# Optimization experiments

Hardware: AMD Instinct MI355X
Metric: run time of the kernel (lower is better)

Reference implementation:

```python
import jax, jax.numpy as jnp
import numpy as np

SPATIAL_SHAPES = np.array([[100, 100], [50, 50], [25, 25], [13, 13]], dtype=np.int64)
LEVEL_START = np.concatenate([[0], np.cumsum(SPATIAL_SHAPES[:, 0] * SPATIAL_SHAPES[:, 1])[:-1]])
L_TOK = int((SPATIAL_SHAPES[:, 0] * SPATIAL_SHAPES[:, 1]).sum())  # 13294
B, D_MODEL, N_HEADS, N_LEVELS, N_POINTS, D_FFN = 4, 256, 8, 4, 4, 1024
HEAD_DIM = D_MODEL // N_HEADS


def setup_inputs() -> dict:
    key = jax.random.key(0)
    ks = jax.random.split(key, 16)
    p = lambda k, s: jax.random.normal(k, s, jnp.float32) * 0.02
    return {
        'src': jax.random.normal(ks[0], (B, L_TOK, D_MODEL), jnp.float32),
        'src2': jax.random.normal(ks[1], (B, L_TOK, D_MODEL), jnp.float32),
        'pos': jax.random.normal(ks[2], (B, L_TOK, D_MODEL), jnp.float32),
        'memory_pos': jax.random.normal(ks[3], (B, L_TOK, D_MODEL), jnp.float32),
        'value_w': p(ks[4], (D_MODEL, D_MODEL)), 'value_b': jnp.zeros((D_MODEL,), jnp.float32),
        'off_w': p(ks[5], (D_MODEL, N_HEADS * N_LEVELS * N_POINTS * 2)),
        'off_b': p(ks[6], (N_HEADS * N_LEVELS * N_POINTS * 2,)),
        'aw_w': p(ks[7], (D_MODEL, N_HEADS * N_LEVELS * N_POINTS)),
        'aw_b': jnp.zeros((N_HEADS * N_LEVELS * N_POINTS,), jnp.float32),
        'out_w': p(ks[8], (D_MODEL, D_MODEL)), 'out_b': jnp.zeros((D_MODEL,), jnp.float32),
        'ln_g': jnp.ones((D_MODEL,), jnp.float32), 'ln_b': jnp.zeros((D_MODEL,), jnp.float32),
        'lin1_w': p(ks[9], (D_MODEL, D_FFN)), 'lin1_b': jnp.zeros((D_FFN,), jnp.float32),
        'lin2_w': p(ks[10], (D_FFN, D_MODEL)), 'lin2_b': jnp.zeros((D_MODEL,), jnp.float32),
    }


def _layer_norm(x, g, b, eps=1e-5):
    mu = jnp.mean(x, -1, keepdims=True)
    var = jnp.mean(jnp.square(x - mu), -1, keepdims=True)
    return (x - mu) * jax.lax.rsqrt(var + eps) * g + b


def _reference_points():
    # per get_reference_points: normalized (x, y) centers per src level -> [1, L_TOK, 1, 2]
    pts = []
    for H_, W_ in SPATIAL_SHAPES:
        ry, rx = np.meshgrid(np.linspace(0.5, H_ - 0.5, H_) / H_,
                             np.linspace(0.5, W_ - 0.5, W_) / W_, indexing='ij')
        pts.append(np.stack([rx.reshape(-1), ry.reshape(-1)], -1))
    return jnp.asarray(np.concatenate(pts, 0), jnp.float32)[None, :, None, :]


def _bilinear(value, loc, H_, W_):
    # value: [N, H*W, D]; loc: [N, S, 2] normalized in [0,1]
    # matches F.grid_sample(align_corners=False, padding_mode='zeros') with grid = 2*loc-1
    x = loc[..., 0] * W_ - 0.5
    y = loc[..., 1] * H_ - 0.5
    x0 = jnp.floor(x)
    y0 = jnp.floor(y)
    wx1 = x - x0
    wy1 = y - y0
    out = jnp.zeros(value.shape[:1] + loc.shape[1:2] + value.shape[2:], value.dtype)
    for dy, wy in ((0, 1.0 - wy1), (1, wy1)):
        for dx, wx in ((0, 1.0 - wx1), (1, wx1)):
            xi = x0 + dx
            yi = y0 + dy
            valid = (xi >= 0) & (xi < W_) & (yi >= 0) & (yi < H_)
            idx = (jnp.clip(yi, 0, H_ - 1) * W_ + jnp.clip(xi, 0, W_ - 1)).astype(jnp.int32)
            v = jnp.take_along_axis(value, idx[..., None], axis=1)
            out = out + v * (wx * wy * valid)[..., None]
    return out


def _ms_deform_attn(query, ref, memory, value_w, value_b, off_w, off_b, aw_w, aw_b, out_w, out_b):
    Bq, Lq = query.shape[0], query.shape[1]
    value = (memory @ value_w + value_b).reshape(Bq, -1, N_HEADS, HEAD_DIM)
    offs = (query @ off_w + off_b).reshape(Bq, Lq, N_HEADS, N_LEVELS, N_POINTS, 2)
    norm = jnp.asarray(SPATIAL_SHAPES[:, ::-1].copy(), jnp.float32)  # (W, H) per level
    loc = ref[:, :, None, :, None, :] + offs / norm[None, None, None, :, None, :]
    aw = jax.nn.softmax((query @ aw_w + aw_b).reshape(Bq, Lq, N_HEADS, N_LEVELS * N_POINTS), -1)
    aw = aw.reshape(Bq, Lq, N_HEADS, N_LEVELS, N_POINTS)
    acc = jnp.zeros((Bq, Lq, N_HEADS, HEAD_DIM), query.dtype)
    for l in range(N_LEVELS):
        H_, W_ = int(SPATIAL_SHAPES[l, 0]), int(SPATIAL_SHAPES[l, 1])
        s = int(LEVEL_START[l])
        v = value[:, s:s + H_ * W_].transpose(0, 2, 1, 3).reshape(Bq * N_HEADS, H_ * W_, HEAD_DIM)
        ll = loc[:, :, :, l].transpose(0, 2, 1, 3, 4).reshape(Bq * N_HEADS, Lq * N_POINTS, 2)
        samp = _bilinear(v, ll, H_, W_).reshape(Bq, N_HEADS, Lq, N_POINTS, HEAD_DIM)
        acc = acc + jnp.einsum('bhqpd,bqhp->bqhd', samp, aw[:, :, :, l])
    return acc.reshape(Bq, Lq, D_MODEL) @ out_w + out_b


def reference(src, src2, pos, memory_pos, value_w, value_b, off_w, off_b, aw_w, aw_b,
              out_w, out_b, ln_g, ln_b, lin1_w, lin1_b, lin2_w, lin2_b):
    ref = _reference_points()
    q = src + pos
    mem = src2 + memory_pos
    attn = _ms_deform_attn(q, ref, mem, value_w, value_b, off_w, off_b, aw_w, aw_b, out_w, out_b)
    # residual + norm2 (dropout is identity in eval)
    x = _layer_norm(src + attn, ln_g, ln_b)
    # FFN; note the original re-uses norm2 (it was assigned twice in __init__)
    ffn = jax.nn.relu(x @ lin1_w + lin1_b) @ lin2_w + lin2_b
    return _layer_norm(x + ffn, ln_g, ln_b)
```

## Files before the change

kernel.cpp:

```cpp
#include <hip/hip_runtime.h>
#include <math.h>

#define L_TOKN 13294
#define BATCHN 4
#define NTOK (BATCHN * L_TOKN)
#define NTOKP 53248
#define DMODEL 256
#define DFFN 1024

typedef __attribute__((ext_vector_type(8))) short short8;
typedef __attribute__((ext_vector_type(4))) float f32x4;
typedef __attribute__((ext_vector_type(2))) float f32x2;

__device__ __forceinline__ ushort f2b(float f) {
    uint u = __float_as_uint(f);
    u += 0x7fff + ((u >> 16) & 1);
    return (ushort)(u >> 16);
}
__device__ __forceinline__ float b2f(uint h) {
    return __uint_as_float(h << 16);
}

__global__ __launch_bounds__(256) void prep_k(
    const float* __restrict__ s1, const float* __restrict__ p1,
    const float* __restrict__ s2, const float* __restrict__ p2,
    ushort* __restrict__ o1, ushort* __restrict__ o2,
    const float* __restrict__ w0, const float* __restrict__ w1,
    const float* __restrict__ w2, const float* __restrict__ w3,
    const float* __restrict__ w4, const float* __restrict__ w5,
    ushort* __restrict__ wtb, int n4)
{
    int i = blockIdx.x * 256 + threadIdx.x;
    if (i < 2 * n4) {
        const float* a; const float* b; ushort* o; int j;
        if (i < n4) { a = s1; b = p1; o = o1; j = i; }
        else        { a = s2; b = p2; o = o2; j = i - n4; }
        float4 va = ((const float4*)a)[j];
        float4 vb = ((const float4*)b)[j];
        ushort4 r;
        r.x = f2b(va.x + vb.x); r.y = f2b(va.y + vb.y);
        r.z = f2b(va.z + vb.z); r.w = f2b(va.w + vb.w);
        ((ushort4*)o)[j] = r;
        return;
    }
    int i2 = i - 2 * n4;
    const float* w; int Nd; size_t off; int j;
    if      (i2 < 65536)  { w = w0; Nd = 256;  off = 0;      j = i2; }
    else if (i2 < 131072) { w = w1; Nd = 256;  off = 65536;  j = i2 - 65536; }
    else if (i2 < 163840) { w = w2; Nd = 128;  off = 131072; j = i2 - 131072; }
    else if (i2 < 229376) { w = w3; Nd = 256;  off = 163840; j = i2 - 163840; }
    else if (i2 < 491520) { w = w4; Nd = 1024; off = 229376; j = i2 - 229376; }
    else if (i2 < 753664) { w = w5; Nd = 256;  off = 491520; j = i2 - 491520; }
    else return;
    int Kd = (i2 < 491520) ? 256 : 1024;
    int k = j / Nd, n = j - k * Nd;
    wtb[off + (size_t)n * Kd + k] = f2b(w[j]);
}

__device__ __forceinline__ void gemm_core(
    const ushort* __restrict__ A, const ushort* __restrict__ Wt,
    const float* __restrict__ bias, const float* __restrict__ bias2,
    float* __restrict__ Cf, ushort* __restrict__ Cb,
    int M, int N, int K, int relu, int nsplit, int m0, int n0)
{
    __shared__ ushort lds[16384];

    const int t  = threadIdx.x;
    const int wv = t >> 6, ln_ = t & 63;
    const int wr = wv >> 1, wc = wv & 1;
    const int fr = ln_ & 15;
    const int kg = ln_ >> 4;

    f32x4 acc[4][4];
    #pragma unroll
    for (int i = 0; i < 4; i++)
        #pragma unroll
        for (int j = 0; j < 4; j++) acc[i][j] = (f32x4)0.0f;

    int aoff[4], boff[4];
    #pragma unroll
    for (int i = 0; i < 4; i++) {
        aoff[i] = (wr * 64 + i * 16 + fr) * 32 + kg * 8;
        boff[i] = 4096 + (wc * 64 + i * 16 + fr) * 32 + kg * 8;
    }

#define STAGE(pbuf, k0) do {                                                       \
    _Pragma("unroll")                                                              \
    for (int ii = 0; ii < 2; ii++) {                                               \
        int c = (wv * 2 + ii) * 64 + ln_;                                          \
        int m = c >> 2, s = c & 3;                                                 \
        const ushort* sa = A  + (size_t)(m0 + m) * K + (k0) + s * 8;               \
        const ushort* sb = Wt + (size_t)(n0 + m) * K + (k0) + s * 8;               \
        __builtin_amdgcn_global_load_lds(                                          \
            (const __attribute__((address_space(1))) unsigned int*)sa,             \
            (__attribute__((address_space(3))) unsigned int*)&lds[(pbuf) * 8192 + (wv * 2 + ii) * 512], \
            16, 0, 0);                                                             \
        __builtin_amdgcn_global_load_lds(                                          \
            (const __attribute__((address_space(1))) unsigned int*)sb,             \
            (__attribute__((address_space(3))) unsigned int*)&lds[(pbuf) * 8192 + 4096 + (wv * 2 + ii) * 512], \
            16, 0, 0);                                                             \
    }                                                                              \
} while (0)

    const int nk = K >> 5;
    STAGE(0, 0);
    if (nk > 1) STAGE(1, 32);

    for (int ks = 0; ks < nk; ks++) {
        const int p = ks & 1;
        if (ks + 1 < nk) {
            asm volatile("s_waitcnt vmcnt(4)" ::: "memory");
        } else {
            asm volatile("s_waitcnt vmcnt(0)" ::: "memory");
        }
        __builtin_amdgcn_s_barrier();
        __builtin_amdgcn_sched_barrier(0);

        short8 af[4], bf[4];
        const int pb = p * 8192;
        #pragma unroll
        for (int i = 0; i < 4; i++) {
            af[i] = *(const short8*)&lds[pb + aoff[i]];
            bf[i] = *(const short8*)&lds[pb + boff[i]];
        }
        if (ks + 2 < nk) {
            asm volatile("s_waitcnt lgkmcnt(0)" ::: "memory");
            __builtin_amdgcn_s_barrier();
            __builtin_amdgcn_sched_barrier(0);
            STAGE(p, (ks + 2) << 5);
        }
        #pragma unroll
        for (int i = 0; i < 4; i++)
            #pragma unroll
            for (int j = 0; j < 4; j++)
                acc[i][j] = __builtin_amdgcn_mfma_f32_16x16x32_bf16(af[i], bf[j], acc[i][j], 0, 0, 0);
    }
#undef STAGE

    #pragma unroll
    for (int i = 0; i < 4; i++) {
        #pragma unroll
        for (int j = 0; j < 4; j++) {
            int col = n0 + wc * 64 + j * 16 + fr;
            float bv = (col < nsplit) ? bias[col] : bias2[col - nsplit];
            #pragma unroll
            for (int e = 0; e < 4; e++) {
                int row = m0 + wr * 64 + i * 16 + kg * 4 + e;
                if (row >= M) continue;
                float v = acc[i][j][e] + bv;
                if (relu) v = fmaxf(v, 0.f);
                if (Cf) Cf[(size_t)row * N + col] = v;
                if (Cb) Cb[(size_t)row * N + col] = f2b(v);
            }
        }
    }
}

__global__ __launch_bounds__(256) void mgemm_k(
    const ushort* __restrict__ A, const ushort* __restrict__ Wt,
    const float* __restrict__ bias, const float* __restrict__ bias2,
    float* __restrict__ Cf, ushort* __restrict__ Cb,
    int M, int N, int K, int relu, int nsplit)
{
    gemm_core(A, Wt, bias, bias2, Cf, Cb, M, N, K, relu, nsplit,
              blockIdx.y * 128, blockIdx.x * 128);
}

__global__ __launch_bounds__(256) void projs_k(
    const ushort* __restrict__ memb, const ushort* __restrict__ qb,
    const ushort* __restrict__ value_wt, const ushort* __restrict__ offaw_wt,
    const float* __restrict__ value_b, const float* __restrict__ off_b,
    const float* __restrict__ aw_b,
    ushort* __restrict__ vb, ushort* __restrict__ offawb)
{
    const int x = blockIdx.x;
    const int m0 = blockIdx.y * 128;
    const ushort* A; const ushort* Wt; const float* b1; const float* b2;
    ushort* Cb; int N, n0;
    if (x < 2) { A = memb; Wt = value_wt; b1 = value_b; b2 = value_b;
                 Cb = vb; N = 256; n0 = x * 128; }
    else       { A = qb;   Wt = offaw_wt; b1 = off_b;   b2 = aw_b;
                 Cb = offawb; N = 384; n0 = (x - 2) * 128; }
    gemm_core(A, Wt, b1, b2, nullptr, Cb, NTOK, N, 256, 0, 256, m0, n0);
}

__global__ __launch_bounds__(256) void deform_k(
    const ushort* __restrict__ Vb,
    const ushort* __restrict__ OFFAW,
    ushort* __restrict__ OUTb)
{
    __shared__ uint4 pw_idx[4][2][136];
    __shared__ uint2 pw_w[4][2][136];

    const int t = threadIdx.x;
    const int wv = t >> 6, lane = t & 63;
    const int tok0 = blockIdx.x * 8 + wv * 2;

    const int HWc[4] = {100, 50, 25, 13};
    const int STc[4] = {0, 10000, 12500, 13125};

    const int ppb = lane & 15;
    const int lvb = ppb >> 2;
    #pragma unroll
    for (int it = 0; it < 4; it++) {
        int tk = it >> 1;
        int h  = ((it & 1) << 2) + (lane >> 4);
        int row = tok0 + tk;
        int b = row / L_TOKN;
        int l = row - b * L_TOKN;
        int st_q, Wq;
        if      (l < 10000) { st_q = 0;     Wq = 100; }
        else if (l < 12500) { st_q = 10000; Wq = 50;  }
        else if (l < 13125) { st_q = 12500; Wq = 25;  }
        else                { st_q = 13125; Wq = 13;  }
        int li = l - st_q;
        int rowi = li / Wq;
        int coli = li - rowi * Wq;
        float rx = (coli + 0.5f) / (float)Wq;
        float ry = (rowi + 0.5f) / (float)Wq;

        const size_t rbase = (size_t)row * 384;
        uint oxy = *(const uint*)(OFFAW + rbase + h * 32 + ppb * 2);
        float ox = b2f(oxy & 0xffffu);
        float oy = b2f(oxy >> 16);
        float lg = b2f((uint)OFFAW[rbase + 256 + h * 16 + ppb]);
        float mx = lg;
        #pragma unroll
        for (int o = 8; o; o >>= 1) mx = fmaxf(mx, __shfl_xor(mx, o));
        float ex = __expf(lg - mx);
        float sm = ex;
        #pragma unroll
        for (int o = 8; o; o >>= 1) sm += __shfl_xor(sm, o);
        float aw = ex / sm;

        int Wl = HWc[lvb], stl = STc[lvb];
        float Wlf = (float)Wl;
        float x = (rx + ox / Wlf) * Wlf - 0.5f;
        float y = (ry + oy / Wlf) * Wlf - 0.5f;
        float x0f = floorf(x), y0f = floorf(y);
        float wx1 = x - x0f, wy1 = y - y0f;
        float wx0 = 1.f - wx1, wy0 = 1.f - wy1;
        int x0 = (int)x0f, y0 = (int)y0f;
        bool vx0 = (x0 >= 0) & (x0 < Wl);
        bool vx1 = (x0 + 1 >= 0) & (x0 + 1 < Wl);
        bool vy0 = (y0 >= 0) & (y0 < Wl);
        bool vy1 = (y0 + 1 >= 0) & (y0 + 1 < Wl);
        int cx0 = min(max(x0, 0), Wl - 1), cx1 = min(max(x0 + 1, 0), Wl - 1);
        int cy0 = min(max(y0, 0), Wl - 1), cy1 = min(max(y0 + 1, 0), Wl - 1);
        uint gb = (uint)(b * L_TOKN + stl);
        uint4 o4;
        o4.x = (gb + cy0 * Wl + cx0) * 512u;
        o4.y = (gb + cy0 * Wl + cx1) * 512u;
        o4.z = (gb + cy1 * Wl + cx0) * 512u;
        o4.w = (gb + cy1 * Wl + cx1) * 512u;
        float w00 = wx0 * wy0 * aw * (float)(vx0 & vy0);
        float w10 = wx1 * wy0 * aw * (float)(vx1 & vy0);
        float w01 = wx0 * wy1 * aw * (float)(vx0 & vy1);
        float w11 = wx1 * wy1 * aw * (float)(vx1 & vy1);
        uint2 wp;
        wp.x = (uint)f2b(w00) | ((uint)f2b(w10) << 16);
        wp.y = (uint)f2b(w01) | ((uint)f2b(w11) << 16);
        pw_idx[wv][tk][h * 17 + ppb] = o4;
        pw_w[wv][tk][h * 17 + ppb]   = wp;
    }

    asm volatile("s_waitcnt lgkmcnt(0)" ::: "memory");
    __builtin_amdgcn_sched_barrier(0);

    const int tk = lane >> 5;
    const int h  = (lane >> 2) & 7;
    const int dq = lane & 3;
    const int row = tok0 + tk;
    const uint choff = (uint)(h * 64 + dq * 16);
    const char* __restrict__ vbase = (const char*)Vb;

    f32x2 acc2[4];
    #pragma unroll
    for (int k = 0; k < 4; k++) acc2[k] = (f32x2)0.0f;

    #pragma unroll 8
    for (int pq = 0; pq < 16; pq++) {
        uint4 o4 = pw_idx[wv][tk][h * 17 + pq];
        uint2 wp = pw_w[wv][tk][h * 17 + pq];
        float w00 = b2f(wp.x & 0xffffu);
        float w10 = __uint_as_float(wp.x & 0xffff0000u);
        float w01 = b2f(wp.y & 0xffffu);
        float w11 = __uint_as_float(wp.y & 0xffff0000u);
        uint4 v00 = *(const uint4*)(vbase + o4.x + choff);
        uint4 v10 = *(const uint4*)(vbase + o4.y + choff);
        uint4 v01 = *(const uint4*)(vbase + o4.z + choff);
        uint4 v11 = *(const uint4*)(vbase + o4.w + choff);
        const uint* p00 = (const uint*)&v00;
        const uint* p10 = (const uint*)&v10;
        const uint* p01 = (const uint*)&v01;
        const uint* p11 = (const uint*)&v11;
        #pragma unroll
        for (int k = 0; k < 4; k++) {
            f32x2 a0, a1, a2, a3;
            a0.x = __uint_as_float(p00[k] << 16); a0.y = __uint_as_float(p00[k] & 0xffff0000u);
            a1.x = __uint_as_float(p10[k] << 16); a1.y = __uint_as_float(p10[k] & 0xffff0000u);
            a2.x = __uint_as_float(p01[k] << 16); a2.y = __uint_as_float(p01[k] & 0xffff0000u);
            a3.x = __uint_as_float(p11[k] << 16); a3.y = __uint_as_float(p11[k] & 0xffff0000u);
            acc2[k] += a0 * w00 + a1 * w10 + a2 * w01 + a3 * w11;
        }
    }
    ushort4 olo, ohi;
    olo.x = f2b(acc2[0].x); olo.y = f2b(acc2[0].y);
    olo.z = f2b(acc2[1].x); olo.w = f2b(acc2[1].y);
    ohi.x = f2b(acc2[2].x); ohi.y = f2b(acc2[2].y);
    ohi.z = f2b(acc2[3].x); ohi.w = f2b(acc2[3].y);
    ushort* op = OUTb + (size_t)row * 256 + h * 32 + dq * 8;
    *(ushort4*)op = olo;
    *(ushort4*)(op + 4) = ohi;
}

__global__ __launch_bounds__(256) void ln_k(
    const float* __restrict__ af, const ushort* __restrict__ ab,
    const float* __restrict__ bf2, const ushort* __restrict__ bb2,
    const float* __restrict__ g, const float* __restrict__ bta,
    float* __restrict__ of, ushort* __restrict__ ob)
{
    const int r = blockIdx.x * 4 + (threadIdx.x >> 6);
    const int lane = threadIdx.x & 63;
    float4 v;
    if (af) {
        v = *((const float4*)(af + (size_t)r * 256) + lane);
    } else {
        ushort4 u = *((const ushort4*)(ab + (size_t)r * 256) + lane);
        v.x = b2f(u.x); v.y = b2f(u.y); v.z = b2f(u.z); v.w = b2f(u.w);
    }
    if (bf2) {
        float4 v2 = *((const float4*)(bf2 + (size_t)r * 256) + lane);
        v.x += v2.x; v.y += v2.y; v.z += v2.z; v.w += v2.w;
    } else if (bb2) {
        ushort4 u = *((const ushort4*)(bb2 + (size_t)r * 256) + lane);
        v.x += b2f(u.x); v.y += b2f(u.y); v.z += b2f(u.z); v.w += b2f(u.w);
    }
    float s = v.x + v.y + v.z + v.w;
    #pragma unroll
    for (int o = 32; o; o >>= 1) s += __shfl_xor(s, o);
    float mu = s * (1.f / 256.f);
    float4 d; d.x = v.x - mu; d.y = v.y - mu; d.z = v.z - mu; d.w = v.w - mu;
    float s2 = d.x * d.x + d.y * d.y + d.z * d.z + d.w * d.w;
    #pragma unroll
    for (int o = 32; o; o >>= 1) s2 += __shfl_xor(s2, o);
    float rstd = rsqrtf(s2 * (1.f / 256.f) + 1e-5f);
    float4 gg = ((const float4*)g)[lane];
    float4 bb = ((const float4*)bta)[lane];
    float4 out;
    out.x = d.x * rstd * gg.x + bb.x;
    out.y = d.y * rstd * gg.y + bb.y;
    out.z = d.z * rstd * gg.z + bb.z;
    out.w = d.w * rstd * gg.w + bb.w;
    if (of) *((float4*)(of + (size_t)r * 256) + lane) = out;
    if (ob) {
        ushort4 o4;
        o4.x = f2b(out.x); o4.y = f2b(out.y); o4.z = f2b(out.z); o4.w = f2b(out.w);
        *((ushort4*)(ob + (size_t)r * 256) + lane) = o4;
    }
}

extern "C" void kernel_launch(void* const* d_in, const int* in_sizes, int n_in,
                              void* d_out, int out_size, void* d_ws, size_t ws_size,
                              hipStream_t stream)
{
    const float* src     = (const float*)d_in[0];
    const float* src2    = (const float*)d_in[1];
    const float* pos     = (const float*)d_in[2];
    const float* mpos    = (const float*)d_in[3];
    const float* value_w = (const float*)d_in[4];
    const float* value_b = (const float*)d_in[5];
    const float* off_w   = (const float*)d_in[6];
    const float* off_b   = (const float*)d_in[7];
    const float* aw_w    = (const float*)d_in[8];
    const float* aw_b    = (const float*)d_in[9];
    const float* out_w   = (const float*)d_in[10];
    const float* out_b   = (const float*)d_in[11];
    const float* ln_g    = (const float*)d_in[12];
    const float* ln_b    = (const float*)d_in[13];
    const float* lin1_w  = (const float*)d_in[14];
    const float* lin1_b  = (const float*)d_in[15];
    const float* lin2_w  = (const float*)d_in[16];
    const float* lin2_b  = (const float*)d_in[17];

    float* outp = (float*)d_out;
    char*  w8   = (char*)d_ws;

    const size_t SLAB = (size_t)NTOKP * 256 * 2;
    const size_t OASZ = (size_t)NTOKP * 384 * 2;
    const size_t HSZ  = (size_t)NTOKP * 1024 * 2;
    ushort* wtb    = (ushort*)(w8);
    ushort* offawb = (ushort*)(w8 + 1572864);
    ushort* qb     = (ushort*)(w8 + 1572864 + OASZ);
    ushort* vb     = (ushort*)(w8 + 1572864 + OASZ + SLAB);
    ushort* memb   = (ushort*)(w8 + 1572864 + HSZ);
    ushort* attb   = (ushort*)(w8 + 1572864 + HSZ + SLAB);

    ushort* hidb   = offawb;
    ushort* bufXb  = memb;
    ushort* projb  = vb;
    ushort* ffn2b  = attb;

    ushort* value_wt = wtb;
    ushort* offaw_wt = wtb + 65536;
    ushort* out_wt   = wtb + 163840;
    ushort* lin1_wt  = wtb + 229376;
    ushort* lin2_wt  = wtb + 491520;

    const dim3 blk(256);
    const int n4 = NTOK * DMODEL / 4;
    const int prep_total = 2 * n4 + 753664;
    prep_k<<<(prep_total + 255) / 256, blk, 0, stream>>>(
        src, pos, src2, mpos, qb, memb,
        value_w, off_w, aw_w, out_w, lin1_w, lin2_w, wtb, n4);

    const int mt = NTOKP / 128;
    projs_k<<<dim3(5, mt), blk, 0, stream>>>(memb, qb, value_wt, offaw_wt,
                                             value_b, off_b, aw_b, vb, offawb);

    deform_k<<<dim3(NTOK / 8), blk, 0, stream>>>(vb, offawb, attb);

    mgemm_k<<<dim3(2, mt), blk, 0, stream>>>(attb, out_wt, out_b, nullptr,
                                             nullptr, projb, NTOK, 256, 256, 0, 256);
    ln_k<<<dim3(NTOK / 4), blk, 0, stream>>>(nullptr, projb, src, nullptr,
                                             ln_g, ln_b, nullptr, bufXb);

    mgemm_k<<<dim3(8, mt), blk, 0, stream>>>(bufXb, lin1_wt, lin1_b, nullptr,
                                             nullptr, hidb, NTOK, DFFN, DMODEL, 1, DFFN);
    mgemm_k<<<dim3(2, mt), blk, 0, stream>>>(hidb, lin2_wt, lin2_b, nullptr,
                                             nullptr, ffn2b, NTOK, DMODEL, DFFN, 0, DMODEL);

    ln_k<<<dim3(NTOK / 4), blk, 0, stream>>>(nullptr, ffn2b, nullptr, bufXb,
                                             ln_g, ln_b, outp, nullptr);
}
```

Before: 419.5 us.

## Shrink GEMM tiles to 64x128 and remap blocks across XCDs

Changes the bf16 MFMA GEMM block tile from 128x128 to 64x128. Each wave now covers 64 rows by 32 columns instead of a 64x64 quadrant, which halves accumulator registers and cuts LDS to 12288 ushorts, and the tile-row grid count doubles. Adds an XCD-aware block index remap so consecutive tiles land on the same chiplet, aiming at better L2 reuse and occupancy. The cost is lower arithmetic intensity per block and more redundant B-tile loads.

```diff
diff --git a/kernel.cpp b/kernel.cpp
--- a/kernel.cpp
+++ b/kernel.cpp
@@ -63,41 +63,45 @@
     float* __restrict__ Cf, ushort* __restrict__ Cb,
     int M, int N, int K, int relu, int nsplit, int m0, int n0)
 {
-    __shared__ ushort lds[16384];
+    __shared__ ushort lds[12288];
 
     const int t  = threadIdx.x;
     const int wv = t >> 6, ln_ = t & 63;
-    const int wr = wv >> 1, wc = wv & 1;
     const int fr = ln_ & 15;
     const int kg = ln_ >> 4;
 
-    f32x4 acc[4][4];
+    f32x4 acc[4][2];
     #pragma unroll
     for (int i = 0; i < 4; i++)
         #pragma unroll
-        for (int j = 0; j < 4; j++) acc[i][j] = (f32x4)0.0f;
-
-    int aoff[4], boff[4];
-    #pragma unroll
-    for (int i = 0; i < 4; i++) {
-        aoff[i] = (wr * 64 + i * 16 + fr) * 32 + kg * 8;
-        boff[i] = 4096 + (wc * 64 + i * 16 + fr) * 32 + kg * 8;
-    }
+        for (int j = 0; j < 2; j++) acc[i][j] = (f32x4)0.0f;
+
+    int aoff[4], boff[2];
+    #pragma unroll
+    for (int i = 0; i < 4; i++)
+        aoff[i] = (i * 16 + fr) * 32 + kg * 8;
+    #pragma unroll
+    for (int j = 0; j < 2; j++)
+        boff[j] = 2048 + (wv * 32 + j * 16 + fr) * 32 + kg * 8;
 
 #define STAGE(pbuf, k0) do {                                                       \
-    _Pragma("unroll")                                                              \
-    for (int ii = 0; ii < 2; ii++) {                                               \
-        int c = (wv * 2 + ii) * 64 + ln_;                                          \
+    {                                                   \
+        int c = wv * 64 + ln_;                                                     \
         int m = c >> 2, s = c & 3;                                                 \
-        const ushort* sa = A  + (size_t)(m0 + m) * K + (k0) + s * 8;               \
-        const ushort* sb = Wt + (size_t)(n0 + m) * K + (k0) + s * 8;               \
+        const ushort* sa = A + (size_t)(m0 + m) * K + (k0) + s * 8;                \
         __builtin_amdgcn_global_load_lds(                                          \
             (const __attribute__((address_space(1))) unsigned int*)sa,             \
-            (__attribute__((address_space(3))) unsigned int*)&lds[(pbuf) * 8192 + (wv * 2 + ii) * 512], \
+            (__attribute__((address_space(3))) unsigned int*)&lds[(pbuf) * 6144 + wv * 512], \
             16, 0, 0);                                                             \
+    }                                                                              \
+    _Pragma("unroll")                                                              \
+    for (int ii = 0; ii < 2; ii++) {                    \
+        int c = wv * 128 + ii * 64 + ln_;                                          \
+        int n = c >> 2, s = c & 3;                                                 \
+        const ushort* sb = Wt + (size_t)(n0 + n) * K + (k0) + s * 8;               \
         __builtin_amdgcn_global_load_lds(                                          \
             (const __attribute__((address_space(1))) unsigned int*)sb,             \
-            (__attribute__((address_space(3))) unsigned int*)&lds[(pbuf) * 8192 + 4096 + (wv * 2 + ii) * 512], \
+            (__attribute__((address_space(3))) unsigned int*)&lds[(pbuf) * 6144 + 2048 + wv * 1024 + ii * 512], \
             16, 0, 0);                                                             \
     }                                                                              \
 } while (0)
@@ -109,20 +113,22 @@
     for (int ks = 0; ks < nk; ks++) {
         const int p = ks & 1;
         if (ks + 1 < nk) {
-            asm volatile("s_waitcnt vmcnt(4)" ::: "memory");
+            asm volatile("s_waitcnt vmcnt(3)" ::: "memory");
         } else {
             asm volatile("s_waitcnt vmcnt(0)" ::: "memory");
         }
         __builtin_amdgcn_s_barrier();
         __builtin_amdgcn_sched_barrier(0);
 
-        short8 af[4], bf[4];
-        const int pb = p * 8192;
-        #pragma unroll
-        for (int i = 0; i < 4; i++) {
+        short8 af[4], bf[2];
+        const int pb = p * 6144;
+        #pragma unroll
+        for (int i = 0; i < 4; i++)
             af[i] = *(const short8*)&lds[pb + aoff[i]];
-            bf[i] = *(const short8*)&lds[pb + boff[i]];
-        }
+        #pragma unroll
+        for (int j = 0; j < 2; j++)
+            bf[j] = *(const short8*)&lds[pb + boff[j]];
+
         if (ks + 2 < nk) {
             asm volatile("s_waitcnt lgkmcnt(0)" ::: "memory");
             __builtin_amdgcn_s_barrier();
@@ -132,7 +138,7 @@
         #pragma unroll
         for (int i = 0; i < 4; i++)
             #pragma unroll
-            for (int j = 0; j < 4; j++)
+            for (int j = 0; j < 2; j++)
                 acc[i][j] = __builtin_amdgcn_mfma_f32_16x16x32_bf16(af[i], bf[j], acc[i][j], 0, 0, 0);
     }
 #undef STAGE
@@ -140,12 +146,12 @@
     #pragma unroll
     for (int i = 0; i < 4; i++) {
         #pragma unroll
-        for (int j = 0; j < 4; j++) {
-            int col = n0 + wc * 64 + j * 16 + fr;
+        for (int j = 0; j < 2; j++) {
+            int col = n0 + wv * 32 + j * 16 + fr;
             float bv = (col < nsplit) ? bias[col] : bias2[col - nsplit];
             #pragma unroll
             for (int e = 0; e < 4; e++) {
-                int row = m0 + wr * 64 + i * 16 + kg * 4 + e;
+                int row = m0 + i * 16 + kg * 4 + e;
                 if (row >= M) continue;
                 float v = acc[i][j][e] + bv;
                 if (relu) v = fmaxf(v, 0.f);
@@ -156,14 +162,26 @@
     }
 }
 
+__device__ __forceinline__ int2 xcd_tile(int nx)
+{
+    int flat  = blockIdx.x + blockIdx.y * gridDim.x;
+    int total = gridDim.x * gridDim.y;
+    int tile;
+    if (total & 7) tile = flat;
+    else           tile = (flat & 7) * (total >> 3) + (flat >> 3);
+    int2 r; r.x = tile % nx; r.y = tile / nx;
+    return r;
+}
+
 __global__ __launch_bounds__(256) void mgemm_k(
     const ushort* __restrict__ A, const ushort* __restrict__ Wt,
     const float* __restrict__ bias, const float* __restrict__ bias2,
     float* __restrict__ Cf, ushort* __restrict__ Cb,
     int M, int N, int K, int relu, int nsplit)
 {
+    int2 xy = xcd_tile(gridDim.x);
     gemm_core(A, Wt, bias, bias2, Cf, Cb, M, N, K, relu, nsplit,
-              blockIdx.y * 128, blockIdx.x * 128);
+              xy.y * 64, xy.x * 128);
 }
 
 __global__ __launch_bounds__(256) void projs_k(
@@ -173,15 +191,15 @@
     const float* __restrict__ aw_b,
     ushort* __restrict__ vb, ushort* __restrict__ offawb)
 {
-    const int x = blockIdx.x;
-    const int m0 = blockIdx.y * 128;
-    const ushort* A; const ushort* Wt; const float* b1; const float* b2;
-    ushort* Cb; int N, n0;
-    if (x < 2) { A = memb; Wt = value_wt; b1 = value_b; b2 = value_b;
-                 Cb = vb; N = 256; n0 = x * 128; }
-    else       { A = qb;   Wt = offaw_wt; b1 = off_b;   b2 = aw_b;
-                 Cb = offawb; N = 384; n0 = (x - 2) * 128; }
-    gemm_core(A, Wt, b1, b2, nullptr, Cb, NTOK, N, 256, 0, 256, m0, n0);
+    int2 xy = xcd_tile(5);
+    const int x = xy.x;
+    const int m0 = xy.y * 64;
+    if (x < 2)
+        gemm_core(memb, value_wt, value_b, value_b, nullptr, vb,
+                  NTOK, 256, 256, 0, 256, m0, x * 128);
+    else
+        gemm_core(qb, offaw_wt, off_b, aw_b, nullptr, offawb,
+                  NTOK, 384, 256, 0, 256, m0, (x - 2) * 128);
 }
 
 __global__ __launch_bounds__(256) void deform_k(
@@ -414,7 +432,7 @@
         src, pos, src2, mpos, qb, memb,
         value_w, off_w, aw_w, out_w, lin1_w, lin2_w, wtb, n4);
 
-    const int mt = NTOKP / 128;
+    const int mt = NTOKP / 64;
     projs_k<<<dim3(5, mt), blk, 0, stream>>>(memb, qb, value_wt, offaw_wt,
                                              value_b, off_b, aw_b, vb, offawb);
 
```

Measured after the change: 362.7 us. 13.5% less time.
